# Kernel optimization log

Hardware: AMD Instinct MI355X
Metric: run time of the kernel (lower is better)

Reference implementation:

```python
import jax, jax.numpy as jnp
import numpy as np

B, T, DH, DS, A = 32, 2048, 1024, 1024, 512

def setup_inputs() -> dict:
    key = jax.random.key(0)
    k1, k2, k3, k4, k5 = jax.random.split(key, 5)
    s = jax.random.normal(k1, (B, DS), dtype=jnp.float32)
    h = jax.random.normal(k2, (B, T, DH), dtype=jnp.float32)
    # glorot_uniform for W_a, U_a; uniform(-0.05, 0.05) for v_a (Keras defaults)
    lim_W = np.sqrt(6.0 / (DS + A)).astype(np.float32)
    lim_U = np.sqrt(6.0 / (DH + A)).astype(np.float32)
    W_a = jax.random.uniform(k3, (DS, A), minval=-lim_W, maxval=lim_W, dtype=jnp.float32)
    U_a = jax.random.uniform(k4, (DH, A), minval=-lim_U, maxval=lim_U, dtype=jnp.float32)
    v_a = jax.random.uniform(k5, (A,), minval=-0.05, maxval=0.05, dtype=jnp.float32)
    return {"s": s, "h": h, "W_a": W_a, "U_a": U_a, "v_a": v_a}

def reference(s, h, W_a, U_a, v_a):
    # U_a_h: [B, T, A]; W_a_s: [B, 1, A]
    U_a_h = jnp.einsum('btd,da->bta', h, U_a)
    W_a_s = (s @ W_a)[:, None, :]
    e = jnp.tanh(W_a_s + U_a_h)          # [B, T, A]
    e = jnp.einsum('bta,a->bt', e, v_a)   # learned-vector reduction
    a = jax.nn.softmax(e, axis=-1)        # exp / sum over time (same math, stable)
    c = jnp.einsum('bt,btd->bd', a, h)    # weighted sum over time
    return c
```

## Files before the change

kernel.cpp:

```cpp
#include <hip/hip_runtime.h>
#include <hip/hip_bf16.h>

#define B_  32
#define T_  2048
#define DH_ 1024
#define DS_ 1024
#define A_  512
#define M_  (B_ * T_)
#define NCH 16

typedef __attribute__((ext_vector_type(8))) short bf16x8;
typedef __attribute__((ext_vector_type(4))) float f32x4;

__device__ __forceinline__ unsigned short f2bf(float f) {
    union { float f; unsigned u; } v; v.f = f;
    unsigned r = 0x7FFFu + ((v.u >> 16) & 1u);
    return (unsigned short)((v.u + r) >> 16);
}
__device__ __forceinline__ float fast_tanh(float x) {
    float cx = fminf(fmaxf(x, -9.f), 9.f);
    float e2 = __expf(2.f * cx);
    return (e2 - 1.f) / (e2 + 1.f);
}
__device__ __forceinline__ unsigned pack_bf2(float lo, float hi) {
    union { float f; unsigned u; } a, b;
    a.f = lo; b.f = hi;
    return __builtin_amdgcn_perm(b.u + 0x8000u, a.u + 0x8000u, 0x07060302u);
}

__global__ void prep_ut(const float* __restrict__ U, unsigned short* __restrict__ Ut) {
    int o = blockIdx.x * 256 + threadIdx.x;
    int a = o >> 10, k = o & (DH_ - 1);
    Ut[o] = f2bf(U[k * A_ + a]);
}

__global__ void ws_gemv2(const float* __restrict__ s, const float* __restrict__ W,
                         float* __restrict__ Ws) {
    __shared__ float red[4][64];
    const int blk = blockIdx.x;
    const int b = blk >> 3, a0 = (blk & 7) * 64;
    const int tid = threadIdx.x;
    const int a = a0 + (tid & 63), kq = tid >> 6;
    const float* sp = s + b * DS_ + kq * 256;
    const float* wp = W + (size_t)(kq * 256) * A_ + a;
    float acc = 0.f;
#pragma unroll 8
    for (int k = 0; k < 256; ++k) acc += sp[k] * wp[(size_t)k * A_];
    red[kq][tid & 63] = acc;
    __syncthreads();
    if (tid < 64)
        Ws[b * A_ + a0 + tid] = red[0][tid] + red[1][tid] + red[2][tid] + red[3][tid];
}

__global__ void __launch_bounds__(512, 2)
fused_reg(const float* __restrict__ h,
          const unsigned short* __restrict__ Ut,
          const float* __restrict__ Ws, const float* __restrict__ va,
          float* __restrict__ pm, float* __restrict__ pl,
          float* __restrict__ pc) {
    __shared__ unsigned short As[2][128][32];

    const int tid = threadIdx.x;
    const int tm = blockIdx.x;
    const int rowBase = tm * 128;

    const int lane = tid & 63;
    const int wid = tid >> 6;
    const int wm = wid >> 2, wn = wid & 3;
    const int lr = lane & 15, kg = lane >> 4;
    const int gsw16 = (kg ^ ((lr >> 1) & 3)) * 8;

    const int ar = tid >> 2;
    const int alg = tid & 3;

    f32x4 acc[4][8];
#pragma unroll
    for (int i = 0; i < 4; ++i)
#pragma unroll
        for (int j = 0; j < 8; ++j) acc[i][j] = (f32x4){0.f, 0.f, 0.f, 0.f};

    auto loadA = [&](float4* areg, int t) {
        const float* hp = h + (size_t)(rowBase + ar) * DH_ + t * 32 + alg * 8;
        areg[0] = *(const float4*)(hp);
        areg[1] = *(const float4*)(hp + 4);
    };
    const unsigned short* bbase = Ut + (size_t)(wn * 128 + lr) * DH_ + kg * 8;
    auto loadB = [&](bf16x8* bq, int t) {
        const unsigned short* bp = bbase + t * 32;
#pragma unroll
        for (int nf = 0; nf < 8; ++nf)
            bq[nf] = *(const bf16x8*)(bp + (size_t)nf * 16 * DH_);
    };
    auto packwriteA = [&](const float4* areg, int buf) {
        uint4 u;
        u.x = pack_bf2(areg[0].x, areg[0].y);
        u.y = pack_bf2(areg[0].z, areg[0].w);
        u.z = pack_bf2(areg[1].x, areg[1].y);
        u.w = pack_bf2(areg[1].z, areg[1].w);
        int p = alg ^ ((ar >> 1) & 3);
        *(uint4*)((char*)&As[buf][0][0] + ar * 64 + p * 16) = u;
    };

    float4 areg0[2], areg1[2];
    bf16x8 bq0[8], bq1[8];
    const int NT = DH_ / 32;

    loadA(areg0, 0);
    __builtin_amdgcn_sched_barrier(0);
    loadA(areg1, 1);
    __builtin_amdgcn_sched_barrier(0);
    loadB(bq0, 0);
    __builtin_amdgcn_sched_barrier(0);
    packwriteA(areg0, 0);
    asm volatile("s_waitcnt lgkmcnt(0)" ::: "memory");
    __builtin_amdgcn_s_barrier();
    __builtin_amdgcn_sched_barrier(0);

#define KSTEP(T_, BQ_C, BQ_N, AR_C, AR_N)                                     \
    {                                                                         \
        const int t_ = (T_);                                                  \
        loadA(AR_N, t_ + 2);                                                  \
        __builtin_amdgcn_sched_barrier(0);                                    \
        loadB(BQ_N, t_ + 1);                                                  \
        __builtin_amdgcn_sched_barrier(0);                                    \
        bf16x8 af[4];                                                         \
        const unsigned short* Ab = &As[t_ & 1][0][0];                         \
        _Pragma("unroll")                                                     \
        for (int mi = 0; mi < 4; ++mi)                                        \
            af[mi] = *(const bf16x8*)(Ab + (wm * 64 + mi * 16 + lr) * 32 + gsw16); \
        __builtin_amdgcn_s_setprio(1);                                        \
        _Pragma("unroll")                                                     \
        for (int mi = 0; mi < 4; ++mi)                                        \
            _Pragma("unroll")                                                 \
            for (int nf = 0; nf < 8; ++nf)                                    \
                acc[mi][nf] = __builtin_amdgcn_mfma_f32_16x16x32_bf16(        \
                    af[mi], BQ_C[nf], acc[mi][nf], 0, 0, 0);                  \
        __builtin_amdgcn_s_setprio(0);                                        \
        __builtin_amdgcn_sched_barrier(0);                                    \
        packwriteA(AR_C, (t_ + 1) & 1);                                       \
        asm volatile("s_waitcnt lgkmcnt(0)" ::: "memory");                    \
        __builtin_amdgcn_s_barrier();                                         \
        __builtin_amdgcn_sched_barrier(0);                                    \
    }

#pragma unroll 1
    for (int t = 0; t < NT - 2; t += 2) {
        KSTEP(t, bq0, bq1, areg1, areg0);
        KSTEP(t + 1, bq1, bq0, areg0, areg1);
    }
    {
        loadB(bq1, NT - 1);
        __builtin_amdgcn_sched_barrier(0);
        bf16x8 af[4];
        const unsigned short* Ab = &As[(NT - 2) & 1][0][0];
#pragma unroll
        for (int mi = 0; mi < 4; ++mi)
            af[mi] = *(const bf16x8*)(Ab + (wm * 64 + mi * 16 + lr) * 32 + gsw16);
#pragma unroll
        for (int mi = 0; mi < 4; ++mi)
#pragma unroll
            for (int nf = 0; nf < 8; ++nf)
                acc[mi][nf] = __builtin_amdgcn_mfma_f32_16x16x32_bf16(
                    af[mi], bq0[nf], acc[mi][nf], 0, 0, 0);
        packwriteA(areg1, (NT - 1) & 1);
        asm volatile("s_waitcnt lgkmcnt(0)" ::: "memory");
        __builtin_amdgcn_s_barrier();
        __builtin_amdgcn_sched_barrier(0);
    }
    {
        bf16x8 af[4];
        const unsigned short* Ab = &As[(NT - 1) & 1][0][0];
#pragma unroll
        for (int mi = 0; mi < 4; ++mi)
            af[mi] = *(const bf16x8*)(Ab + (wm * 64 + mi * 16 + lr) * 32 + gsw16);
#pragma unroll
        for (int mi = 0; mi < 4; ++mi)
#pragma unroll
            for (int nf = 0; nf < 8; ++nf)
                acc[mi][nf] = __builtin_amdgcn_mfma_f32_16x16x32_bf16(
                    af[mi], bq1[nf], acc[mi][nf], 0, 0, 0);
    }
    __syncthreads();

    float* er_s  = (float*)&As[0][0][0];
    float* red_s = er_s + 128;
    float* w_s   = er_s + 256;
    float* pf    = er_s + 384;

    const int bIdx = rowBase >> 11;
    const float* WsRow = Ws + bIdx * A_;
    float wsv[8], vav[8];
#pragma unroll
    for (int nf = 0; nf < 8; ++nf) {
        int a = wn * 128 + nf * 16 + lr;
        wsv[nf] = WsRow[a];
        vav[nf] = va[a];
    }
#pragma unroll
    for (int mi = 0; mi < 4; ++mi) {
#pragma unroll
        for (int j = 0; j < 4; ++j) {
            float ssum = 0.f;
#pragma unroll
            for (int nf = 0; nf < 8; ++nf) {
                float x = acc[mi][nf][j] + wsv[nf];
                ssum += fast_tanh(x) * vav[nf];
            }
            ssum += __shfl_xor(ssum, 1);
            ssum += __shfl_xor(ssum, 2);
            ssum += __shfl_xor(ssum, 4);
            ssum += __shfl_xor(ssum, 8);
            if (lr == 0) {
                int r = wm * 64 + mi * 16 + kg * 4 + j;
                pf[r * 4 + wn] = ssum;
            }
        }
    }
    __syncthreads();
    if (tid < 128) {
        float v = pf[tid * 4] + pf[tid * 4 + 1] + pf[tid * 4 + 2] + pf[tid * 4 + 3];
        er_s[tid] = v;
        red_s[tid] = v;
    }
    __syncthreads();
    if (tid < 64) red_s[tid] = fmaxf(red_s[tid], red_s[tid + 64]);
    __syncthreads();
    if (tid < 32) red_s[tid] = fmaxf(red_s[tid], red_s[tid + 32]);
    __syncthreads();
    if (tid < 16) red_s[tid] = fmaxf(red_s[tid], red_s[tid + 16]);
    __syncthreads();
    if (tid < 8) red_s[tid] = fmaxf(red_s[tid], red_s[tid + 8]);
    __syncthreads();
    if (tid < 4) red_s[tid] = fmaxf(red_s[tid], red_s[tid + 4]);
    __syncthreads();
    if (tid < 2) red_s[tid] = fmaxf(red_s[tid], red_s[tid + 2]);
    __syncthreads();
    if (tid == 0) red_s[0] = fmaxf(red_s[0], red_s[1]);
    __syncthreads();
    const float mloc = red_s[0];
    __syncthreads();
    if (tid < 128) {
        float w = __expf(er_s[tid] - mloc);
        w_s[tid] = w;
        red_s[tid] = w;
    }
    __syncthreads();
    if (tid < 64) red_s[tid] += red_s[tid + 64];
    __syncthreads();
    if (tid < 32) red_s[tid] += red_s[tid + 32];
    __syncthreads();
    if (tid < 16) red_s[tid] += red_s[tid + 16];
    __syncthreads();
    if (tid < 8) red_s[tid] += red_s[tid + 8];
    __syncthreads();
    if (tid < 4) red_s[tid] += red_s[tid + 4];
    __syncthreads();
    if (tid < 2) red_s[tid] += red_s[tid + 2];
    __syncthreads();
    if (tid == 0) {
        pm[tm] = mloc;
        pl[tm] = red_s[0] + red_s[1];
    }

    float c0 = 0.f, c1 = 0.f;
    const float* hp = h + (size_t)rowBase * DH_ + tid;
#pragma unroll 4
    for (int t = 0; t < 128; ++t) {
        float w = w_s[t];
        c0 += w * hp[(size_t)t * DH_];
        c1 += w * hp[(size_t)t * DH_ + 512];
    }
    float* pcp = pc + (size_t)tm * DH_;
    pcp[tid] = c0;
    pcp[tid + 512] = c1;
}

__global__ void combine(const float* __restrict__ pm, const float* __restrict__ pl,
                        const float* __restrict__ pc, float* __restrict__ c) {
    const int b = blockIdx.x;
    const int tid = threadIdx.x;
    float M = -1e30f;
#pragma unroll
    for (int i = 0; i < NCH; ++i) M = fmaxf(M, pm[b * NCH + i]);
    float L = 0.f;
    float sc[NCH];
#pragma unroll
    for (int i = 0; i < NCH; ++i) {
        sc[i] = __expf(pm[b * NCH + i] - M);
        L += sc[i] * pl[b * NCH + i];
    }
    float a0 = 0.f, a1 = 0.f;
#pragma unroll
    for (int i = 0; i < NCH; ++i) {
        const float* pcp = pc + (size_t)(b * NCH + i) * DH_;
        a0 += sc[i] * pcp[tid];
        a1 += sc[i] * pcp[tid + 512];
    }
    const float inv = 1.f / L;
    c[(size_t)b * DH_ + tid] = a0 * inv;
    c[(size_t)b * DH_ + tid + 512] = a1 * inv;
}

extern "C" void kernel_launch(void* const* d_in, const int* in_sizes, int n_in,
                              void* d_out, int out_size, void* d_ws, size_t ws_size,
                              hipStream_t stream) {
    const float* s   = (const float*)d_in[0];
    const float* h   = (const float*)d_in[1];
    const float* W_a = (const float*)d_in[2];
    const float* U_a = (const float*)d_in[3];
    const float* v_a = (const float*)d_in[4];
    float* c = (float*)d_out;

    float* Ws = (float*)d_ws;
    unsigned short* Ut = (unsigned short*)(Ws + B_ * A_);
    float* pm = (float*)(Ut + (size_t)A_ * DH_);
    float* pl = pm + B_ * NCH;
    float* pc = pl + B_ * NCH;

    prep_ut<<<(A_ * DH_) / 256, 256, 0, stream>>>(U_a, Ut);
    ws_gemv2<<<B_ * 8, 256, 0, stream>>>(s, W_a, Ws);
    fused_reg<<<B_ * NCH, 512, 0, stream>>>(h, Ut, Ws, v_a, pm, pl, pc);
    combine<<<B_, 512, 0, stream>>>(pm, pl, pc, c);
}
```

Before: 215.1 us.

## Load A fragments directly from global into registers, dropping LDS staging

The GEMM main loop no longer stages h through shared memory. Each wave now loads its own fp32 rows of h straight into registers, packs them to bf16 and feeds them to MFMA, with B fragments double-buffered in registers. This removes the LDS writes and reads and the per-k-step barriers. In exchange, the 4 waves that share a row block each reload the same h rows from global memory, which is four times the A traffic through L2. It also adds register pressure and removes the explicit sched_barrier ordering.

After: 348.7 us. 1.62x slower.

```diff
diff --git a/kernel.cpp b/kernel.cpp
--- a/kernel.cpp
+++ b/kernel.cpp
@@ -53,12 +53,12 @@
 }
 
 __global__ void __launch_bounds__(512, 2)
-fused_reg(const float* __restrict__ h,
-          const unsigned short* __restrict__ Ut,
-          const float* __restrict__ Ws, const float* __restrict__ va,
-          float* __restrict__ pm, float* __restrict__ pl,
-          float* __restrict__ pc) {
-    __shared__ unsigned short As[2][128][32];
+fused_direct(const float* __restrict__ h,
+             const unsigned short* __restrict__ Ut,
+             const float* __restrict__ Ws, const float* __restrict__ va,
+             float* __restrict__ pm, float* __restrict__ pl,
+             float* __restrict__ pc) {
+    __shared__ float smem[896];
 
     const int tid = threadIdx.x;
     const int tm = blockIdx.x;
@@ -68,10 +68,6 @@
     const int wid = tid >> 6;
     const int wm = wid >> 2, wn = wid & 3;
     const int lr = lane & 15, kg = lane >> 4;
-    const int gsw16 = (kg ^ ((lr >> 1) & 3)) * 8;
-
-    const int ar = tid >> 2;
-    const int alg = tid & 3;
 
     f32x4 acc[4][8];
 #pragma unroll
@@ -79,55 +75,48 @@
 #pragma unroll
         for (int j = 0; j < 8; ++j) acc[i][j] = (f32x4){0.f, 0.f, 0.f, 0.f};
 
-    auto loadA = [&](float4* areg, int t) {
-        const float* hp = h + (size_t)(rowBase + ar) * DH_ + t * 32 + alg * 8;
-        areg[0] = *(const float4*)(hp);
-        areg[1] = *(const float4*)(hp + 4);
+    const float* abase = h + (size_t)(rowBase + wm * 64 + lr) * DH_ + kg * 8;
+    const unsigned short* bbase = Ut + (size_t)(wn * 128 + lr) * DH_ + kg * 8;
+
+    auto loadAf32 = [&](float4* at, int t) {
+#pragma unroll
+        for (int mi = 0; mi < 4; ++mi) {
+            const float* p = abase + (size_t)mi * 16 * DH_ + t * 32;
+            at[2 * mi]     = *(const float4*)p;
+            at[2 * mi + 1] = *(const float4*)(p + 4);
+        }
     };
-    const unsigned short* bbase = Ut + (size_t)(wn * 128 + lr) * DH_ + kg * 8;
+    auto packA = [&](const float4* at, bf16x8* af) {
+#pragma unroll
+        for (int mi = 0; mi < 4; ++mi) {
+            union { bf16x8 v; uint4 u; } q;
+            q.u.x = pack_bf2(at[2 * mi].x, at[2 * mi].y);
+            q.u.y = pack_bf2(at[2 * mi].z, at[2 * mi].w);
+            q.u.z = pack_bf2(at[2 * mi + 1].x, at[2 * mi + 1].y);
+            q.u.w = pack_bf2(at[2 * mi + 1].z, at[2 * mi + 1].w);
+            af[mi] = q.v;
+        }
+    };
     auto loadB = [&](bf16x8* bq, int t) {
         const unsigned short* bp = bbase + t * 32;
 #pragma unroll
         for (int nf = 0; nf < 8; ++nf)
             bq[nf] = *(const bf16x8*)(bp + (size_t)nf * 16 * DH_);
     };
-    auto packwriteA = [&](const float4* areg, int buf) {
-        uint4 u;
-        u.x = pack_bf2(areg[0].x, areg[0].y);
-        u.y = pack_bf2(areg[0].z, areg[0].w);
-        u.z = pack_bf2(areg[1].x, areg[1].y);
-        u.w = pack_bf2(areg[1].z, areg[1].w);
-        int p = alg ^ ((ar >> 1) & 3);
-        *(uint4*)((char*)&As[buf][0][0] + ar * 64 + p * 16) = u;
-    };
-
-    float4 areg0[2], areg1[2];
-    bf16x8 bq0[8], bq1[8];
+
+    float4 at[8];
+    bf16x8 af[4], bq0[8], bq1[8];
     const int NT = DH_ / 32;
 
-    loadA(areg0, 0);
-    __builtin_amdgcn_sched_barrier(0);
-    loadA(areg1, 1);
-    __builtin_amdgcn_sched_barrier(0);
+    loadAf32(at, 0);
     loadB(bq0, 0);
-    __builtin_amdgcn_sched_barrier(0);
-    packwriteA(areg0, 0);
-    asm volatile("s_waitcnt lgkmcnt(0)" ::: "memory");
-    __builtin_amdgcn_s_barrier();
-    __builtin_amdgcn_sched_barrier(0);
-
-#define KSTEP(T_, BQ_C, BQ_N, AR_C, AR_N)                                     \
+    loadB(bq1, 1);
+
+#define KSTEP(T_, BQ_C)                                                       \
     {                                                                         \
         const int t_ = (T_);                                                  \
-        loadA(AR_N, t_ + 2);                                                  \
-        __builtin_amdgcn_sched_barrier(0);                                    \
-        loadB(BQ_N, t_ + 1);                                                  \
-        __builtin_amdgcn_sched_barrier(0);                                    \
-        bf16x8 af[4];                                                         \
-        const unsigned short* Ab = &As[t_ & 1][0][0];                         \
-        _Pragma("unroll")                                                     \
-        for (int mi = 0; mi < 4; ++mi)                                        \
-            af[mi] = *(const bf16x8*)(Ab + (wm * 64 + mi * 16 + lr) * 32 + gsw16); \
+        packA(at, af);                                                        \
+        if (t_ + 1 < NT) loadAf32(at, t_ + 1);                                \
         __builtin_amdgcn_s_setprio(1);                                        \
         _Pragma("unroll")                                                     \
         for (int mi = 0; mi < 4; ++mi)                                        \
@@ -136,56 +125,20 @@
                 acc[mi][nf] = __builtin_amdgcn_mfma_f32_16x16x32_bf16(        \
                     af[mi], BQ_C[nf], acc[mi][nf], 0, 0, 0);                  \
         __builtin_amdgcn_s_setprio(0);                                        \
-        __builtin_amdgcn_sched_barrier(0);                                    \
-        packwriteA(AR_C, (t_ + 1) & 1);                                       \
-        asm volatile("s_waitcnt lgkmcnt(0)" ::: "memory");                    \
-        __builtin_amdgcn_s_barrier();                                         \
-        __builtin_amdgcn_sched_barrier(0);                                    \
+        if (t_ + 2 < NT) loadB(BQ_C, t_ + 2);                                 \
     }
 
 #pragma unroll 1
-    for (int t = 0; t < NT - 2; t += 2) {
-        KSTEP(t, bq0, bq1, areg1, areg0);
-        KSTEP(t + 1, bq1, bq0, areg0, areg1);
-    }
-    {
-        loadB(bq1, NT - 1);
-        __builtin_amdgcn_sched_barrier(0);
-        bf16x8 af[4];
-        const unsigned short* Ab = &As[(NT - 2) & 1][0][0];
-#pragma unroll
-        for (int mi = 0; mi < 4; ++mi)
-            af[mi] = *(const bf16x8*)(Ab + (wm * 64 + mi * 16 + lr) * 32 + gsw16);
-#pragma unroll
-        for (int mi = 0; mi < 4; ++mi)
-#pragma unroll
-            for (int nf = 0; nf < 8; ++nf)
-                acc[mi][nf] = __builtin_amdgcn_mfma_f32_16x16x32_bf16(
-                    af[mi], bq0[nf], acc[mi][nf], 0, 0, 0);
-        packwriteA(areg1, (NT - 1) & 1);
-        asm volatile("s_waitcnt lgkmcnt(0)" ::: "memory");
-        __builtin_amdgcn_s_barrier();
-        __builtin_amdgcn_sched_barrier(0);
-    }
-    {
-        bf16x8 af[4];
-        const unsigned short* Ab = &As[(NT - 1) & 1][0][0];
-#pragma unroll
-        for (int mi = 0; mi < 4; ++mi)
-            af[mi] = *(const bf16x8*)(Ab + (wm * 64 + mi * 16 + lr) * 32 + gsw16);
-#pragma unroll
-        for (int mi = 0; mi < 4; ++mi)
-#pragma unroll
-            for (int nf = 0; nf < 8; ++nf)
-                acc[mi][nf] = __builtin_amdgcn_mfma_f32_16x16x32_bf16(
-                    af[mi], bq1[nf], acc[mi][nf], 0, 0, 0);
-    }
-    __syncthreads();
-
-    float* er_s  = (float*)&As[0][0][0];
-    float* red_s = er_s + 128;
-    float* w_s   = er_s + 256;
-    float* pf    = er_s + 384;
+    for (int t = 0; t < NT; t += 2) {
+        KSTEP(t, bq0);
+        KSTEP(t + 1, bq1);
+    }
+#undef KSTEP
+
+    float* er_s  = smem;
+    float* red_s = smem + 128;
+    float* w_s   = smem + 256;
+    float* pf    = smem + 384;
 
     const int bIdx = rowBase >> 11;
     const float* WsRow = Ws + bIdx * A_;
@@ -319,6 +272,6 @@
 
     prep_ut<<<(A_ * DH_) / 256, 256, 0, stream>>>(U_a, Ut);
     ws_gemv2<<<B_ * 8, 256, 0, stream>>>(s, W_a, Ws);
-    fused_reg<<<B_ * NCH, 512, 0, stream>>>(h, Ut, Ws, v_a, pm, pl, pc);
+    fused_direct<<<B_ * NCH, 512, 0, stream>>>(h, Ut, Ws, v_a, pm, pl, pc);
     combine<<<B_, 512, 0, stream>>>(pm, pl, pc, c);
 }
```
